# Performance work log

Measured on AMD Instinct MI355X. Metric: run time of the kernel, lower is better.

The kernel has to match this reference:

```python
import jax, jax.numpy as jnp
import numpy as np
import math

DEPTH = 2
RATIOS = (0.5, 0.5)
K_PROP = 2  # Gra_inc(2)


def _prop(x, ei, ew, K=K_PROP):
    # GCN-style sym-normalized diffusion with implicit self-loops; Gra_inc(K)
    N = x.shape[0]
    row, col = ei[0], ei[1]
    deg = jax.ops.segment_sum(ew, row, num_segments=N) + 1.0  # +1 self-loop
    dinv = jax.lax.rsqrt(deg)
    norm = dinv[row] * ew * dinv[col]          # [E]
    self_n = (dinv * dinv)[:, None]            # [N,1]
    h, out = x, x
    for _ in range(K):
        h = jax.ops.segment_sum(norm[:, None] * h[col], row, num_segments=N) + self_n * h
        out = out + h
    return out


def _conv(x, ei, ew, W):
    return _prop(x @ W, ei, ew)


def _pool(x, ei, ew, pw, ratio):
    # PyG TopKPooling: score = tanh(x.pw/||pw||), keep top ceil(ratio*N) nodes,
    # gate features by score, relabel surviving edges (dropped edges -> weight 0).
    N = x.shape[0]
    k = int(math.ceil(ratio * N))
    score = jnp.tanh(x @ pw / jnp.linalg.norm(pw))
    val, perm = jax.lax.top_k(score, k)
    x2 = x[perm] * val[:, None]
    nm = jnp.full((N,), -1, jnp.int32).at[perm].set(jnp.arange(k, dtype=jnp.int32))
    r, c = nm[ei[0]], nm[ei[1]]
    kept = (r >= 0) & (c >= 0)
    ei2 = jnp.stack([jnp.where(kept, r, 0), jnp.where(kept, c, 0)])
    ew2 = jnp.where(kept, ew, 0.0)
    return x2, ei2, ew2, perm


def setup_inputs() -> dict:
    key = jax.random.key(0)
    ks = jax.random.split(key, 10)
    N, E, C_in, C_hid, C_out = 50000, 800000, 128, 128, 64
    def w(k, i, o):
        return jax.random.normal(k, (i, o), jnp.float32) / np.sqrt(i)
    return {
        "x": jax.random.normal(ks[0], (N, C_in), jnp.float32),
        "edge_index": jax.random.randint(ks[1], (2, E), 0, N, dtype=jnp.int32),
        "Wd0": w(ks[2], C_in, C_hid),
        "Wd1": w(ks[3], C_hid, C_hid),
        "Wd2": w(ks[4], C_hid, C_hid),
        "pw0": jax.random.normal(ks[5], (C_hid,), jnp.float32) / np.sqrt(C_hid),
        "pw1": jax.random.normal(ks[6], (C_hid,), jnp.float32) / np.sqrt(C_hid),
        "Wu0": w(ks[7], C_hid, C_hid),
        "Wu1": w(ks[8], C_hid, C_hid),
        "Wu2": w(ks[9], 2 * C_hid, C_out),
    }


def reference(x, edge_index, Wd0, Wd1, Wd2, pw0, pw1, Wu0, Wu1, Wu2):
    ei = edge_index
    ew = jnp.ones((ei.shape[1],), x.dtype)
    x = jax.nn.relu(_conv(x, ei, ew, Wd0))
    org = x
    xs, eis, ews, perms = [x], [ei], [ew], []
    for i, (pw, Wd) in enumerate(zip((pw0, pw1), (Wd1, Wd2))):
        x, ei, ew, perm = _pool(x, ei, ew, pw, RATIOS[i])
        x = jax.nn.relu(_conv(x, ei, ew, Wd))
        if i < DEPTH - 1:
            xs.append(x); eis.append(ei); ews.append(ew)
        perms.append(perm)
    for i, Wu in enumerate((Wu0, Wu1)):
        j = DEPTH - 1 - i
        res, ei, ew, perm = xs[j], eis[j], ews[j], perms[j]
        up = jnp.zeros_like(res).at[perm].set(x)
        x = res + up  # sum_res skip fusion
        x = _conv(x, ei, ew, Wu)
        if i < DEPTH - 1:
            x = jax.nn.relu(x)
    x = jnp.concatenate([x, org], axis=1)
    return _conv(x, ei, ew, Wu2)
```

## Files before the change

### kernel.cpp

```cpp
#include <hip/hip_runtime.h>
#include <hip/hip_bf16.h>
#include <stdint.h>

#define DEV __device__ __forceinline__

static constexpr int C_HID = 128;

DEV float4 f4_fma(float a, float4 w, float4 acc) {
  acc.x = fmaf(a, w.x, acc.x); acc.y = fmaf(a, w.y, acc.y);
  acc.z = fmaf(a, w.z, acc.z); acc.w = fmaf(a, w.w, acc.w);
  return acc;
}

__global__ void scorekeys_kernel(const float* __restrict__ x, const float* __restrict__ pw,
                                 float* __restrict__ score, unsigned long long* __restrict__ keys,
                                 int N) {
  int row = blockIdx.x * 4 + (threadIdx.x >> 6);
  int lane = threadIdx.x & 63;
  if (row >= N) return;
  float p0 = pw[lane], p1 = pw[lane + 64];
  float pn = p0 * p0 + p1 * p1;
  const float* xr = x + (size_t)row * C_HID;
  float s = xr[lane] * p0 + xr[lane + 64] * p1;
#pragma unroll
  for (int o = 32; o > 0; o >>= 1) {
    s += __shfl_xor(s, o, 64);
    pn += __shfl_xor(pn, o, 64);
  }
  if (lane == 0) {
    float sc = tanhf(s / sqrtf(pn));
    score[row] = sc;
    unsigned u = __float_as_uint(sc);
    u ^= (u >> 31) ? 0xFFFFFFFFu : 0x80000000u;
    keys[row] = (((unsigned long long)(~u)) << 16) | (unsigned)row;
  }
}

__global__ void select_init_kernel(unsigned long long* prefix, int* rem, int k, int* hist3) {
  int i = blockIdx.x * 256 + threadIdx.x;
  if (i == 0) { *prefix = 0ull; *rem = k; }
  for (int j = i; j < 3 * 65536; j += gridDim.x * 256) hist3[j] = 0;
}

__global__ void select_hist_kernel(const unsigned long long* __restrict__ keys, int N,
                                   const unsigned long long* __restrict__ prefix,
                                   int shift, unsigned long long M, int* __restrict__ hist) {
  int i = blockIdx.x * 256 + threadIdx.x;
  if (i >= N) return;
  unsigned long long P = *prefix;
  unsigned long long key = keys[i];
  if (((key ^ P) & M) == 0)
    atomicAdd(&hist[(int)((key >> shift) & 0xFFFF)], 1);
}

__global__ void select_find_kernel(const int* __restrict__ hist,
                                   unsigned long long* __restrict__ prefix,
                                   int* __restrict__ rem, int shift, int* __restrict__ ctr) {
  int t = threadIdx.x;
  int base = t * 64;
  int s = 0;
#pragma unroll
  for (int j = 0; j < 64; ++j) s += hist[base + j];
  int lane = t & 63, w = t >> 6;
  int v = s;
  for (int o = 1; o < 64; o <<= 1) { int u = __shfl_up(v, o, 64); if (lane >= o) v += u; }
  __shared__ int ws[16];
  if (lane == 63) ws[w] = v;
  __syncthreads();
  if (t < 16) {
    int u = ws[t];
    for (int o = 1; o < 16; o <<= 1) { int uu = __shfl_up(u, o, 64); if (t >= o) u += uu; }
    ws[t] = u;
  }
  __syncthreads();
  int incl = v + (w > 0 ? ws[w - 1] : 0);
  int excl = incl - s;
  int R = *rem;
  if (excl < R && incl >= R) {
    int c = excl, b = base;
    for (int j = 0; j < 64; ++j) {
      int h = hist[base + j];
      if (c + h >= R) { b = base + j; break; }
      c += h;
    }
    *prefix |= ((unsigned long long)b) << shift;
    *rem = R - c;
    if (shift == 0) *ctr = 0;
  }
}

__global__ void select_enum_kernel(const unsigned long long* __restrict__ keys, int N,
                                   const unsigned long long* __restrict__ Tptr,
                                   int* __restrict__ ctr, int* __restrict__ perm,
                                   int* __restrict__ nm) {
  int i = blockIdx.x * 256 + threadIdx.x;
  if (i >= N) return;
  unsigned long long T = *Tptr;
  if (keys[i] <= T) { int r = atomicAdd(ctr, 1); perm[r] = i; nm[i] = r; }
  else nm[i] = -1;
}

__global__ void pool_gather_kernel(const float* __restrict__ xold, const float* __restrict__ score,
                                   const int* __restrict__ perm, float* __restrict__ xnew, int k) {
  int j = blockIdx.x * 2 + (threadIdx.x >> 7);
  int f = threadIdx.x & 127;
  if (j >= k) return;
  int src = perm[j];
  xnew[(size_t)j * C_HID + f] = xold[(size_t)src * C_HID + f] * score[src];
}

DEV bool map_edge(int a, int b, const int* m0, const int* m1, int& r, int& c) {
  r = a; c = b;
  if (m0) { r = m0[r]; c = m0[c]; if ((r | c) < 0) return false; }
  if (m1) { r = m1[r]; c = m1[c]; if ((r | c) < 0) return false; }
  return true;
}

__global__ void edge_count_kernel(const int* __restrict__ ei, int E, int* __restrict__ cnt) {
  int e = blockIdx.x * 256 + threadIdx.x;
  if (e >= E) return;
  atomicAdd(&cnt[ei[e]], 1);
}

__global__ void edge_fill_kernel(const int* __restrict__ ei, int E,
                                 const int* __restrict__ rowptr, int* __restrict__ fc,
                                 int* __restrict__ colv) {
  int e = blockIdx.x * 256 + threadIdx.x;
  if (e >= E) return;
  int r = ei[e], c = ei[E + e];
  int pos = rowptr[r] + atomicAdd(&fc[r], 1);
  colv[pos] = c;
}

#define CEPT 7
__global__ __launch_bounds__(1024) void edge_count_compact_kernel(
    const int* __restrict__ ei, int E, const int* m0, const int* m1,
    int* __restrict__ cnt, int2* __restrict__ pairs, int* __restrict__ pctr) {
  int tid = threadIdx.x;
  int gbase = blockIdx.x * (1024 * CEPT) + tid;
  int rs[CEPT], cs[CEPT];
  int myn = 0;
#pragma unroll
  for (int i = 0; i < CEPT; ++i) {
    int e = gbase + i * 1024;
    int r, c;
    bool keep = (e < E) && map_edge(ei[e], ei[E + e], m0, m1, r, c);
    rs[i] = keep ? r : -1;
    cs[i] = keep ? c : 0;
    if (keep) { atomicAdd(&cnt[r], 1); ++myn; }
  }
  int lane = tid & 63, w = tid >> 6;
  int v = myn;
  for (int o = 1; o < 64; o <<= 1) { int u = __shfl_up(v, o, 64); if (lane >= o) v += u; }
  __shared__ int ws[16];
  __shared__ int bbase;
  if (lane == 63) ws[w] = v;
  __syncthreads();
  if (tid < 16) {
    int u = ws[tid];
    for (int o = 1; o < 16; o <<= 1) { int uu = __shfl_up(u, o, 64); if (tid >= o) u += uu; }
    ws[tid] = u;
  }
  __syncthreads();
  int excl = v - myn + (w > 0 ? ws[w - 1] : 0);
  if (tid == 1023) bbase = atomicAdd(pctr, excl + myn);
  __syncthreads();
  int pos = bbase + excl;
#pragma unroll
  for (int i = 0; i < CEPT; ++i)
    if (rs[i] >= 0) pairs[pos++] = make_int2(rs[i], cs[i]);
}

__global__ void edge_fill_compact_kernel(const int2* __restrict__ pairs, const int* __restrict__ pctr,
                                         const int* __restrict__ rowptr, int* __restrict__ fc,
                                         int* __restrict__ colv) {
  int i = blockIdx.x * 256 + threadIdx.x;
  if (i >= *pctr) return;
  int2 pr = pairs[i];
  int pos = rowptr[pr.x] + atomicAdd(&fc[pr.x], 1);
  colv[pos] = pr.y;
}

__global__ void scan_partial_kernel(const int* __restrict__ cnt, int n, int* __restrict__ bsum) {
  int i = blockIdx.x * 256 + threadIdx.x;
  int v = (i < n) ? cnt[i] : 0;
#pragma unroll
  for (int o = 32; o > 0; o >>= 1) v += __shfl_down(v, o, 64);
  __shared__ int ws[4];
  if ((threadIdx.x & 63) == 0) ws[threadIdx.x >> 6] = v;
  __syncthreads();
  if (threadIdx.x == 0) bsum[blockIdx.x] = ws[0] + ws[1] + ws[2] + ws[3];
}

__global__ void scan_blocksums_kernel(int* __restrict__ bsum, int nb) {
  int t = threadIdx.x;
  int v = (t < nb) ? bsum[t] : 0;
  int lane = t & 63, w = t >> 6;
  for (int o = 1; o < 64; o <<= 1) { int u = __shfl_up(v, o, 64); if (lane >= o) v += u; }
  __shared__ int ws[16];
  if (lane == 63) ws[w] = v;
  __syncthreads();
  if (t < 16) {
    int u = ws[t];
    for (int o = 1; o < 16; o <<= 1) { int uu = __shfl_up(u, o, 64); if (t >= o) u += uu; }
    ws[t] = u;
  }
  __syncthreads();
  if (t < nb) bsum[t] = v + (w > 0 ? ws[w - 1] : 0);
}

__global__ void scan_scatter_kernel(const int* __restrict__ cnt, int n,
                                    const int* __restrict__ bsum,
                                    int* __restrict__ rowptr, float* __restrict__ dinv,
                                    int* __restrict__ fc) {
  int i = blockIdx.x * 256 + threadIdx.x;
  int v = (i < n) ? cnt[i] : 0;
  int lane = threadIdx.x & 63, w = threadIdx.x >> 6;
  int s = v;
  for (int o = 1; o < 64; o <<= 1) { int u = __shfl_up(s, o, 64); if (lane >= o) s += u; }
  __shared__ int ws[4];
  __shared__ int wo[4];
  if (lane == 63) ws[w] = s;
  __syncthreads();
  if (threadIdx.x == 0) { int c = 0; for (int j = 0; j < 4; ++j) { wo[j] = c; c += ws[j]; } }
  __syncthreads();
  int excl = s - v + wo[w] + (blockIdx.x > 0 ? bsum[blockIdx.x - 1] : 0);
  if (i < n) {
    rowptr[i] = excl;
    dinv[i] = rsqrtf((float)v + 1.0f);
    fc[i] = 0;
    if (i == n - 1) rowptr[n] = excl + v;
  }
}

template <int FIRST, int RELU>
__global__ void spmm_kernel(const int* __restrict__ rowptr, const int* __restrict__ colv,
                            const float* __restrict__ dinv,
                            const float* __restrict__ h_in, const float* __restrict__ x0,
                            float* __restrict__ out, int M, int C) {
  int lanes = C >> 2;
  int rpb = 256 / lanes;
  int r = blockIdx.x * rpb + (int)threadIdx.x / lanes;
  int lane = (int)threadIdx.x % lanes;
  if (r >= M) return;
  float d = dinv[r];
  const float4* hin4 = (const float4*)h_in;
  size_t base = (size_t)r * lanes + lane;
  float4 self = hin4[base];
  float sn = d * d;
  float4 v = make_float4(sn * self.x, sn * self.y, sn * self.z, sn * self.w);
  int e0 = rowptr[r], e1 = rowptr[r + 1];
  int e = e0;
  for (; e + 4 <= e1; e += 4) {
    int c0 = colv[e], c1 = colv[e + 1], c2 = colv[e + 2], c3 = colv[e + 3];
    float4 h0 = hin4[(size_t)c0 * lanes + lane];
    float4 h1 = hin4[(size_t)c1 * lanes + lane];
    float4 h2 = hin4[(size_t)c2 * lanes + lane];
    float4 h3 = hin4[(size_t)c3 * lanes + lane];
    float w0 = d * dinv[c0], w1 = d * dinv[c1], w2 = d * dinv[c2], w3 = d * dinv[c3];
    v = f4_fma(w0, h0, v);
    v = f4_fma(w1, h1, v);
    v = f4_fma(w2, h2, v);
    v = f4_fma(w3, h3, v);
  }
  for (; e < e1; ++e) {
    int c = colv[e];
    float w = d * dinv[c];
    float4 h = hin4[(size_t)c * lanes + lane];
    v = f4_fma(w, h, v);
  }
  if (FIRST) {
    ((float4*)out)[base] = v;
  } else {
    float4 a = ((const float4*)x0)[base];
    a.x += self.x + v.x; a.y += self.y + v.y; a.z += self.z + v.z; a.w += self.w + v.w;
    if (RELU) { a.x = fmaxf(a.x, 0.f); a.y = fmaxf(a.y, 0.f); a.z = fmaxf(a.z, 0.f); a.w = fmaxf(a.w, 0.f); }
    ((float4*)out)[base] = a;
  }
}

template <int NC, int KT>
__global__ __launch_bounds__(256) void gemm_kernel(const float* __restrict__ A1,
                                                   const float* __restrict__ A2, int K1,
                                                   const float* __restrict__ W,
                                                   float* __restrict__ Cd, int M) {
  constexpr int KTILE = 32;
  constexpr int AP = KTILE + 4;
  constexpr int CG = NC / 4;
  constexpr int RG = 256 / CG;
  constexpr int RPT = 64 / RG;
  __shared__ float Wl[KTILE * NC];
  __shared__ float Al[64 * AP];
  int tid = threadIdx.x;
  int r0 = blockIdx.x * 64;
  int cg = tid % CG, rg = tid / CG;
  float4 acc[RPT];
#pragma unroll
  for (int m = 0; m < RPT; ++m) acc[m] = make_float4(0.f, 0.f, 0.f, 0.f);

  for (int k0 = 0; k0 < KT; k0 += KTILE) {
    const float4* Wg = (const float4*)(W + (size_t)k0 * NC);
    for (int idx = tid; idx < KTILE * NC / 4; idx += 256)
      ((float4*)Wl)[idx] = Wg[idx];
#pragma unroll
    for (int s = 0; s < (64 * KTILE / 4) / 256; ++s) {
      int f4i = tid + s * 256;
      int row = f4i >> 3;
      int kk = (f4i & 7) << 2;
      int gr = r0 + row, gk = k0 + kk;
      float4 v = make_float4(0.f, 0.f, 0.f, 0.f);
      if (gr < M) {
        if (gk < K1) v = *(const float4*)(A1 + (size_t)gr * K1 + gk);
        else         v = *(const float4*)(A2 + (size_t)gr * (KT - K1) + (gk - K1));
      }
      *(float4*)&Al[row * AP + kk] = v;
    }
    __syncthreads();
#pragma unroll
    for (int kk0 = 0; kk0 < KTILE; kk0 += 4) {
      float4 a4[RPT];
#pragma unroll
      for (int m = 0; m < RPT; ++m)
        a4[m] = *(const float4*)&Al[(rg * RPT + m) * AP + kk0];
#pragma unroll
      for (int j = 0; j < 4; ++j) {
        float4 w = *(const float4*)&Wl[(kk0 + j) * NC + cg * 4];
#pragma unroll
        for (int m = 0; m < RPT; ++m) {
          float a = (j == 0) ? a4[m].x : (j == 1) ? a4[m].y : (j == 2) ? a4[m].z : a4[m].w;
          acc[m] = f4_fma(a, w, acc[m]);
        }
      }
    }
    __syncthreads();
  }
#pragma unroll
  for (int m = 0; m < RPT; ++m) {
    int gr = r0 + rg * RPT + m;
    if (gr < M) *(float4*)(Cd + (size_t)gr * NC + cg * 4) = acc[m];
  }
}

__global__ void skip_add_kernel(const float* __restrict__ res, const float* __restrict__ up,
                                const int* __restrict__ nm, float* __restrict__ dst, int n) {
  int idx = blockIdx.x * 256 + threadIdx.x;
  int i = idx >> 5, f4 = idx & 31;
  if (i >= n) return;
  int j = nm[i];
  float4 v = ((const float4*)res)[(size_t)i * 32 + f4];
  if (j >= 0) {
    float4 u = ((const float4*)up)[(size_t)j * 32 + f4];
    v.x += u.x; v.y += u.y; v.z += u.z; v.w += u.w;
  }
  ((float4*)dst)[(size_t)i * 32 + f4] = v;
}

extern "C" void kernel_launch(void* const* d_in, const int* in_sizes, int n_in,
                              void* d_out, int out_size, void* d_ws, size_t ws_size,
                              hipStream_t stream) {
  const float* x   = (const float*)d_in[0];
  const int*   ei  = (const int*)d_in[1];
  const float* Wd0 = (const float*)d_in[2];
  const float* Wd1 = (const float*)d_in[3];
  const float* Wd2 = (const float*)d_in[4];
  const float* pw0 = (const float*)d_in[5];
  const float* pw1 = (const float*)d_in[6];
  const float* Wu0 = (const float*)d_in[7];
  const float* Wu1 = (const float*)d_in[8];
  const float* Wu2 = (const float*)d_in[9];
  float* out = (float*)d_out;

  const int C = C_HID;
  int N0 = in_sizes[0] / C;
  int E  = in_sizes[1] / 2;
  int k1 = (N0 + 1) / 2;
  int k2 = (k1 + 1) / 2;

  char* p = (char*)d_ws;
  auto alloc = [&](size_t bytes) { char* q = p; p += (bytes + 255) & ~(size_t)255; return q; };
  float* org   = (float*)alloc((size_t)N0 * C * 4);
  float* b0    = (float*)alloc((size_t)N0 * C * 4);
  float* b1    = (float*)alloc((size_t)N0 * C * 4);
  float* b2    = (float*)alloc((size_t)N0 * C * 4);
  float* x1res = (float*)alloc((size_t)k1 * C * 4);
  float* score = (float*)alloc((size_t)N0 * 4);
  unsigned long long* keys = (unsigned long long*)alloc((size_t)N0 * 8);
  int* perm0 = (int*)alloc((size_t)k1 * 4);
  int* perm1 = (int*)alloc((size_t)k2 * 4);
  int* map0  = (int*)alloc((size_t)N0 * 4);
  int* map1  = (int*)alloc((size_t)k1 * 4);
  int* cnt   = (int*)alloc((size_t)N0 * 4);
  int* fc    = (int*)alloc((size_t)N0 * 4);
  int* rp0   = (int*)alloc((size_t)(N0 + 1) * 4);
  int* rp1   = (int*)alloc((size_t)(k1 + 1) * 4);
  int* rp2   = (int*)alloc((size_t)(k2 + 1) * 4);
  float* dinv0 = (float*)alloc((size_t)N0 * 4);
  float* dinv1 = (float*)alloc((size_t)k1 * 4);
  float* dinv2 = (float*)alloc((size_t)k2 * 4);
  int* col0 = (int*)alloc((size_t)E * 4);
  int* col1 = (int*)alloc((size_t)E * 4);
  int* col2 = (int*)alloc((size_t)E * 4);
  int2* pairs = (int2*)alloc((size_t)E * 8);
  int* hist3 = (int*)alloc((size_t)3 * 65536 * 4);
  int* bsum = (int*)alloc(1024 * 4);
  unsigned long long* selT = (unsigned long long*)alloc(64);
  int* selRem = (int*)alloc(64);
  int* selCtr = (int*)alloc(64);
  int* pctr = (int*)alloc(64);

  dim3 b256(256);
  int egrid = (E + 255) / 256;
  int cgrid = (E + 1024 * CEPT - 1) / (1024 * CEPT);
  int g0_128 = (N0 + 7) / 8;
  int g1_128 = (k1 + 7) / 8;
  int g2_128 = (k2 + 7) / 8;
  int g0_64  = (N0 + 15) / 16;

  auto scan_csr = [&](int n, int* rowptr, float* dinv) {
    int g = (n + 255) / 256;
    scan_partial_kernel<<<g, b256, 0, stream>>>(cnt, n, bsum);
    scan_blocksums_kernel<<<1, 1024, 0, stream>>>(bsum, g);
    scan_scatter_kernel<<<g, b256, 0, stream>>>(cnt, n, bsum, rowptr, dinv, fc);
  };

  auto topk_select = [&](int N, int k, int* perm, int* nm) {
    int g = (N + 255) / 256;
    select_init_kernel<<<192, b256, 0, stream>>>(selT, selRem, k, hist3);
    int pass = 0;
    for (int shift = 32; shift >= 0; shift -= 16, ++pass) {
      unsigned long long M = (shift == 32) ? 0ull : (~0ull << (shift + 16));
      select_hist_kernel<<<g, b256, 0, stream>>>(keys, N, selT, shift, M, hist3 + pass * 65536);
      select_find_kernel<<<1, 1024, 0, stream>>>(hist3 + pass * 65536, selT, selRem, shift, selCtr);
    }
    select_enum_kernel<<<g, b256, 0, stream>>>(keys, N, selT, selCtr, perm, nm);
  };

  hipMemsetAsync(cnt, 0, (size_t)N0 * 4, stream);
  edge_count_kernel<<<egrid, b256, 0, stream>>>(ei, E, cnt);
  scan_csr(N0, rp0, dinv0);
  edge_fill_kernel<<<egrid, b256, 0, stream>>>(ei, E, rp0, fc, col0);

  gemm_kernel<128, 128><<<(N0 + 63) / 64, b256, 0, stream>>>(x, nullptr, 128, Wd0, b0, N0);
  spmm_kernel<1, 0><<<g0_128, b256, 0, stream>>>(rp0, col0, dinv0, b0, nullptr, b1, N0, 128);
  spmm_kernel<0, 1><<<g0_128, b256, 0, stream>>>(rp0, col0, dinv0, b1, b0, org, N0, 128);

  scorekeys_kernel<<<(N0 + 3) / 4, b256, 0, stream>>>(org, pw0, score, keys, N0);
  topk_select(N0, k1, perm0, map0);
  pool_gather_kernel<<<(k1 + 1) / 2, b256, 0, stream>>>(org, score, perm0, b0, k1);

  hipMemsetAsync(cnt, 0, (size_t)k1 * 4, stream);
  hipMemsetAsync(pctr, 0, 4, stream);
  edge_count_compact_kernel<<<cgrid, 1024, 0, stream>>>(ei, E, map0, nullptr, cnt, pairs, pctr);
  scan_csr(k1, rp1, dinv1);
  edge_fill_compact_kernel<<<egrid, b256, 0, stream>>>(pairs, pctr, rp1, fc, col1);

  gemm_kernel<128, 128><<<(k1 + 63) / 64, b256, 0, stream>>>(b0, nullptr, 128, Wd1, b1, k1);
  spmm_kernel<1, 0><<<g1_128, b256, 0, stream>>>(rp1, col1, dinv1, b1, nullptr, b2, k1, 128);
  spmm_kernel<0, 1><<<g1_128, b256, 0, stream>>>(rp1, col1, dinv1, b2, b1, x1res, k1, 128);

  scorekeys_kernel<<<(k1 + 3) / 4, b256, 0, stream>>>(x1res, pw1, score, keys, k1);
  topk_select(k1, k2, perm1, map1);
  pool_gather_kernel<<<(k2 + 1) / 2, b256, 0, stream>>>(x1res, score, perm1, b0, k2);

  hipMemsetAsync(cnt, 0, (size_t)k2 * 4, stream);
  hipMemsetAsync(pctr, 0, 4, stream);
  edge_count_compact_kernel<<<cgrid, 1024, 0, stream>>>(ei, E, map0, map1, cnt, pairs, pctr);
  scan_csr(k2, rp2, dinv2);
  edge_fill_compact_kernel<<<egrid, b256, 0, stream>>>(pairs, pctr, rp2, fc, col2);

  gemm_kernel<128, 128><<<(k2 + 63) / 64, b256, 0, stream>>>(b0, nullptr, 128, Wd2, b1, k2);
  spmm_kernel<1, 0><<<g2_128, b256, 0, stream>>>(rp2, col2, dinv2, b1, nullptr, b2, k2, 128);
  spmm_kernel<0, 1><<<g2_128, b256, 0, stream>>>(rp2, col2, dinv2, b2, b1, b0, k2, 128);

  skip_add_kernel<<<((size_t)k1 * 32 + 255) / 256, b256, 0, stream>>>(x1res, b0, map1, b2, k1);
  gemm_kernel<128, 128><<<(k1 + 63) / 64, b256, 0, stream>>>(b2, nullptr, 128, Wu0, b1, k1);
  spmm_kernel<1, 0><<<g1_128, b256, 0, stream>>>(rp1, col1, dinv1, b1, nullptr, b0, k1, 128);
  spmm_kernel<0, 1><<<g1_128, b256, 0, stream>>>(rp1, col1, dinv1, b0, b1, b2, k1, 128);

  skip_add_kernel<<<((size_t)N0 * 32 + 255) / 256, b256, 0, stream>>>(org, b2, map0, b0, N0);
  gemm_kernel<128, 128><<<(N0 + 63) / 64, b256, 0, stream>>>(b0, nullptr, 128, Wu1, b1, N0);
  spmm_kernel<1, 0><<<g0_128, b256, 0, stream>>>(rp0, col0, dinv0, b1, nullptr, b2, N0, 128);
  spmm_kernel<0, 0><<<g0_128, b256, 0, stream>>>(rp0, col0, dinv0, b2, b1, b0, N0, 128);

  gemm_kernel<64, 256><<<(N0 + 63) / 64, b256, 0, stream>>>(b0, org, 128, Wu2, b1, N0);
  spmm_kernel<1, 0><<<g0_64, b256, 0, stream>>>(rp0, col0, dinv0, b1, nullptr, b2, N0, 64);
  spmm_kernel<0, 0><<<g0_64, b256, 0, stream>>>(rp0, col0, dinv0, b2, b1, out, N0, 64);
}
```

Baseline: 935.6 us.

## Fold Wu1 into Wu2 and fuse skip-add into GEMM loads

Because the last up-conv has no ReLU and propagation is linear, the code precomputes Wu1 @ Wu2[:128] on device. It then runs the final N0-level diffusion on 64-wide features instead of 128-wide, and adds the org contribution through a second GEMM with a fused add. The skip-add kernels are folded into the GEMM A-tile loads through the node map. The SpMM inner loop also gets an 8-way unrolled path to raise memory-level parallelism. The trade-off is an extra small GEMM and an extra N0 GEMM pass over org, plus floating-point reassociation and higher register pressure in the SpMM.

After: 837.5 us. -10.5%, faster.

```diff
diff --git a/kernel.cpp b/kernel.cpp
--- a/kernel.cpp
+++ b/kernel.cpp
@@ -251,6 +251,19 @@
   float4 v = make_float4(sn * self.x, sn * self.y, sn * self.z, sn * self.w);
   int e0 = rowptr[r], e1 = rowptr[r + 1];
   int e = e0;
+  for (; e + 8 <= e1; e += 8) {
+    int cc[8];
+#pragma unroll
+    for (int i = 0; i < 8; ++i) cc[i] = colv[e + i];
+    float4 hh[8];
+#pragma unroll
+    for (int i = 0; i < 8; ++i) hh[i] = hin4[(size_t)cc[i] * lanes + lane];
+    float ww[8];
+#pragma unroll
+    for (int i = 0; i < 8; ++i) ww[i] = d * dinv[cc[i]];
+#pragma unroll
+    for (int i = 0; i < 8; ++i) v = f4_fma(ww[i], hh[i], v);
+  }
   for (; e + 4 <= e1; e += 4) {
     int c0 = colv[e], c1 = colv[e + 1], c2 = colv[e + 2], c3 = colv[e + 3];
     float4 h0 = hin4[(size_t)c0 * lanes + lane];
@@ -258,10 +271,8 @@
     float4 h2 = hin4[(size_t)c2 * lanes + lane];
     float4 h3 = hin4[(size_t)c3 * lanes + lane];
     float w0 = d * dinv[c0], w1 = d * dinv[c1], w2 = d * dinv[c2], w3 = d * dinv[c3];
-    v = f4_fma(w0, h0, v);
-    v = f4_fma(w1, h1, v);
-    v = f4_fma(w2, h2, v);
-    v = f4_fma(w3, h3, v);
+    v = f4_fma(w0, h0, v); v = f4_fma(w1, h1, v);
+    v = f4_fma(w2, h2, v); v = f4_fma(w3, h3, v);
   }
   for (; e < e1; ++e) {
     int c = colv[e];
@@ -279,11 +290,13 @@
   }
 }
 
-template <int NC, int KT>
-__global__ __launch_bounds__(256) void gemm_kernel(const float* __restrict__ A1,
-                                                   const float* __restrict__ A2, int K1,
+template <int NC, int KT, int SKIP, int ADDIN>
+__global__ __launch_bounds__(256) void gemm_kernel(const float* __restrict__ A1, int K1,
                                                    const float* __restrict__ W,
-                                                   float* __restrict__ Cd, int M) {
+                                                   float* __restrict__ Cd, int M,
+                                                   const float* __restrict__ up,
+                                                   const int* __restrict__ nm,
+                                                   const float* __restrict__ addv) {
   constexpr int KTILE = 32;
   constexpr int AP = KTILE + 4;
   constexpr int CG = NC / 4;
@@ -310,8 +323,14 @@
       int gr = r0 + row, gk = k0 + kk;
       float4 v = make_float4(0.f, 0.f, 0.f, 0.f);
       if (gr < M) {
-        if (gk < K1) v = *(const float4*)(A1 + (size_t)gr * K1 + gk);
-        else         v = *(const float4*)(A2 + (size_t)gr * (KT - K1) + (gk - K1));
+        v = *(const float4*)(A1 + (size_t)gr * K1 + gk);
+        if (SKIP) {
+          int j = nm[gr];
+          if (j >= 0) {
+            float4 u = *(const float4*)(up + (size_t)j * K1 + gk);
+            v.x += u.x; v.y += u.y; v.z += u.z; v.w += u.w;
+          }
+        }
       }
       *(float4*)&Al[row * AP + kk] = v;
     }
@@ -337,22 +356,15 @@
 #pragma unroll
   for (int m = 0; m < RPT; ++m) {
     int gr = r0 + rg * RPT + m;
-    if (gr < M) *(float4*)(Cd + (size_t)gr * NC + cg * 4) = acc[m];
-  }
-}
-
-__global__ void skip_add_kernel(const float* __restrict__ res, const float* __restrict__ up,
-                                const int* __restrict__ nm, float* __restrict__ dst, int n) {
-  int idx = blockIdx.x * 256 + threadIdx.x;
-  int i = idx >> 5, f4 = idx & 31;
-  if (i >= n) return;
-  int j = nm[i];
-  float4 v = ((const float4*)res)[(size_t)i * 32 + f4];
-  if (j >= 0) {
-    float4 u = ((const float4*)up)[(size_t)j * 32 + f4];
-    v.x += u.x; v.y += u.y; v.z += u.z; v.w += u.w;
-  }
-  ((float4*)dst)[(size_t)i * 32 + f4] = v;
+    if (gr < M) {
+      float4 o = acc[m];
+      if (ADDIN) {
+        float4 u = *(const float4*)(addv + (size_t)gr * NC + cg * 4);
+        o.x += u.x; o.y += u.y; o.z += u.z; o.w += u.w;
+      }
+      *(float4*)(Cd + (size_t)gr * NC + cg * 4) = o;
+    }
+  }
 }
 
 extern "C" void kernel_launch(void* const* d_in, const int* in_sizes, int n_in,
@@ -403,6 +415,7 @@
   int2* pairs = (int2*)alloc((size_t)E * 8);
   int* hist3 = (int*)alloc((size_t)3 * 65536 * 4);
   int* bsum = (int*)alloc(1024 * 4);
+  float* Wcat1 = (float*)alloc((size_t)128 * 64 * 4);
   unsigned long long* selT = (unsigned long long*)alloc(64);
   int* selRem = (int*)alloc(64);
   int* selCtr = (int*)alloc(64);
@@ -435,12 +448,14 @@
     select_enum_kernel<<<g, b256, 0, stream>>>(keys, N, selT, selCtr, perm, nm);
   };
 
+  gemm_kernel<64, 128, 0, 0><<<2, b256, 0, stream>>>(Wu1, 128, Wu2, Wcat1, 128, nullptr, nullptr, nullptr);
+
   hipMemsetAsync(cnt, 0, (size_t)N0 * 4, stream);
   edge_count_kernel<<<egrid, b256, 0, stream>>>(ei, E, cnt);
   scan_csr(N0, rp0, dinv0);
   edge_fill_kernel<<<egrid, b256, 0, stream>>>(ei, E, rp0, fc, col0);
 
-  gemm_kernel<128, 128><<<(N0 + 63) / 64, b256, 0, stream>>>(x, nullptr, 128, Wd0, b0, N0);
+  gemm_kernel<128, 128, 0, 0><<<(N0 + 63) / 64, b256, 0, stream>>>(x, 128, Wd0, b0, N0, nullptr, nullptr, nullptr);
   spmm_kernel<1, 0><<<g0_128, b256, 0, stream>>>(rp0, col0, dinv0, b0, nullptr, b1, N0, 128);
   spmm_kernel<0, 1><<<g0_128, b256, 0, stream>>>(rp0, col0, dinv0, b1, b0, org, N0, 128);
 
@@ -454,7 +469,7 @@
   scan_csr(k1, rp1, dinv1);
   edge_fill_compact_kernel<<<egrid, b256, 0, stream>>>(pairs, pctr, rp1, fc, col1);
 
-  gemm_kernel<128, 128><<<(k1 + 63) / 64, b256, 0, stream>>>(b0, nullptr, 128, Wd1, b1, k1);
+  gemm_kernel<128, 128, 0, 0><<<(k1 + 63) / 64, b256, 0, stream>>>(b0, 128, Wd1, b1, k1, nullptr, nullptr, nullptr);
   spmm_kernel<1, 0><<<g1_128, b256, 0, stream>>>(rp1, col1, dinv1, b1, nullptr, b2, k1, 128);
   spmm_kernel<0, 1><<<g1_128, b256, 0, stream>>>(rp1, col1, dinv1, b2, b1, x1res, k1, 128);
 
@@ -468,21 +483,18 @@
   scan_csr(k2, rp2, dinv2);
   edge_fill_compact_kernel<<<egrid, b256, 0, stream>>>(pairs, pctr, rp2, fc, col2);
 
-  gemm_kernel<128, 128><<<(k2 + 63) / 64, b256, 0, stream>>>(b0, nullptr, 128, Wd2, b1, k2);
+  gemm_kernel<128, 128, 0, 0><<<(k2 + 63) / 64, b256, 0, stream>>>(b0, 128, Wd2, b1, k2, nullptr, nullptr, nullptr);
   spmm_kernel<1, 0><<<g2_128, b256, 0, stream>>>(rp2, col2, dinv2, b1, nullptr, b2, k2, 128);
   spmm_kernel<0, 1><<<g2_128, b256, 0, stream>>>(rp2, col2, dinv2, b2, b1, b0, k2, 128);
 
-  skip_add_kernel<<<((size_t)k1 * 32 + 255) / 256, b256, 0, stream>>>(x1res, b0, map1, b2, k1);
-  gemm_kernel<128, 128><<<(k1 + 63) / 64, b256, 0, stream>>>(b2, nullptr, 128, Wu0, b1, k1);
-  spmm_kernel<1, 0><<<g1_128, b256, 0, stream>>>(rp1, col1, dinv1, b1, nullptr, b0, k1, 128);
-  spmm_kernel<0, 1><<<g1_128, b256, 0, stream>>>(rp1, col1, dinv1, b0, b1, b2, k1, 128);
-
-  skip_add_kernel<<<((size_t)N0 * 32 + 255) / 256, b256, 0, stream>>>(org, b2, map0, b0, N0);
-  gemm_kernel<128, 128><<<(N0 + 63) / 64, b256, 0, stream>>>(b0, nullptr, 128, Wu1, b1, N0);
-  spmm_kernel<1, 0><<<g0_128, b256, 0, stream>>>(rp0, col0, dinv0, b1, nullptr, b2, N0, 128);
-  spmm_kernel<0, 0><<<g0_128, b256, 0, stream>>>(rp0, col0, dinv0, b2, b1, b0, N0, 128);
-
-  gemm_kernel<64, 256><<<(N0 + 63) / 64, b256, 0, stream>>>(b0, org, 128, Wu2, b1, N0);
-  spmm_kernel<1, 0><<<g0_64, b256, 0, stream>>>(rp0, col0, dinv0, b1, nullptr, b2, N0, 64);
-  spmm_kernel<0, 0><<<g0_64, b256, 0, stream>>>(rp0, col0, dinv0, b2, b1, out, N0, 64);
-}
+  gemm_kernel<128, 128, 1, 0><<<(k1 + 63) / 64, b256, 0, stream>>>(x1res, 128, Wu0, b1, k1, b0, map1, nullptr);
+  spmm_kernel<1, 0><<<g1_128, b256, 0, stream>>>(rp1, col1, dinv1, b1, nullptr, b2, k1, 128);
+  spmm_kernel<0, 1><<<g1_128, b256, 0, stream>>>(rp1, col1, dinv1, b2, b1, b0, k1, 128);
+
+  gemm_kernel<64, 128, 1, 0><<<(N0 + 63) / 64, b256, 0, stream>>>(org, 128, Wcat1, b2, N0, b0, map0, nullptr);
+  spmm_kernel<1, 0><<<g0_64, b256, 0, stream>>>(rp0, col0, dinv0, b2, nullptr, b1, N0, 64);
+  spmm_kernel<0, 0><<<g0_64, b256, 0, stream>>>(rp0, col0, dinv0, b1, b2, b2, N0, 64);
+  gemm_kernel<64, 128, 0, 1><<<(N0 + 63) / 64, b256, 0, stream>>>(org, 128, Wu2 + (size_t)128 * 64, b0, N0, nullptr, nullptr, b2);
+  spmm_kernel<1, 0><<<g0_64, b256, 0, stream>>>(rp0, col0, dinv0, b0, nullptr, b1, N0, 64);
+  spmm_kernel<0, 0><<<g0_64, b256, 0, stream>>>(rp0, col0, dinv0, b1, b0, out, N0, 64);
+}
```
